# Optimization experiments

Measured on AMD Instinct MI355X. Metric: run time of the kernel, lower is better.

The kernel has to match this reference:

```python
import jax, jax.numpy as jnp
import numpy as np

N_NODES = 100000
N_EDGES = 1600000
IN_CH = 128
OUT_CH = 128
HEADS = 4
HEAD_DIM = OUT_CH // HEADS
NEG_SLOPE_ATT = 0.2   # GATConv default negative_slope
NEG_SLOPE_ACT = 0.2   # block's LeakyReLU(0.2)
BN_EPS = 1e-5


def setup_inputs() -> dict:
    key = jax.random.key(0)
    ks = jax.random.split(key, 6)
    x = jax.random.normal(ks[0], (N_NODES, IN_CH), dtype=jnp.float32)
    edge_index = jax.random.randint(ks[1], (2, N_EDGES), 0, N_NODES, dtype=jnp.int64)
    W = jax.random.normal(ks[2], (IN_CH, HEADS * HEAD_DIM), dtype=jnp.float32) * (1.0 / np.sqrt(IN_CH))
    att_src = jax.random.normal(ks[3], (HEADS, HEAD_DIM), dtype=jnp.float32) * 0.1
    att_dst = jax.random.normal(ks[4], (HEADS, HEAD_DIM), dtype=jnp.float32) * 0.1
    bias = jnp.zeros((OUT_CH,), dtype=jnp.float32)
    gamma = jnp.ones((OUT_CH,), dtype=jnp.float32)
    beta = jnp.zeros((OUT_CH,), dtype=jnp.float32)
    return {"x": x, "edge_index": edge_index, "W": W, "att_src": att_src,
            "att_dst": att_dst, "bias": bias, "gamma": gamma, "beta": beta}


def reference(x, edge_index, W, att_src, att_dst, bias, gamma, beta):
    N = x.shape[0]
    H, C = att_src.shape
    src, dst = edge_index[0], edge_index[1]

    # linear projection per head: [N, H, C]
    h = (x @ W).reshape(N, H, C)

    # per-node attention contributions (alpha_src[i] + alpha_dst[j] on edges)
    a_src = jnp.einsum('nhc,hc->nh', h, att_src)  # [N, H]
    a_dst = jnp.einsum('nhc,hc->nh', h, att_dst)  # [N, H]

    # per-edge raw score, leaky relu (GAT attention nonlinearity)
    e = jax.nn.leaky_relu(a_src[src] + a_dst[dst], NEG_SLOPE_ATT)  # [E, H]

    # segment softmax over edges grouped by destination node
    e_max = jax.ops.segment_max(e, dst, num_segments=N)            # [N, H]
    e_max = jnp.where(jnp.isfinite(e_max), e_max, 0.0)
    ex = jnp.exp(e - e_max[dst])                                   # [E, H]
    denom = jax.ops.segment_sum(ex, dst, num_segments=N)           # [N, H]
    alpha = ex / (denom[dst] + 1e-16)                              # [E, H]

    # scatter-add aggregation of alpha-weighted source features
    msg = alpha[:, :, None] * h[src]                               # [E, H, C]
    out = jax.ops.segment_sum(msg, dst, num_segments=N)            # [N, H, C]
    out = out.reshape(N, H * C) + bias                             # concat heads + bias

    # BatchNorm1d (training mode: batch statistics, biased variance)
    mu = out.mean(axis=0)
    var = out.var(axis=0)
    out = (out - mu) * jax.lax.rsqrt(var + BN_EPS) * gamma + beta

    return jax.nn.leaky_relu(out, NEG_SLOPE_ACT)
```

## Files before the change

### kernel.cpp

```cpp
#include <hip/hip_runtime.h>
#include <hip/hip_fp16.h>
#include <math.h>


#define WAVE  64
#define SHIFT 8
#define CAP   4608
#define CPAD  16

__device__ __forceinline__ float4 leaky4(float4 v, float s) {
    v.x = v.x > 0.f ? v.x : s * v.x;
    v.y = v.y > 0.f ? v.y : s * v.y;
    v.z = v.z > 0.f ? v.z : s * v.z;
    v.w = v.w > 0.f ? v.w : s * v.w;
    return v;
}

__global__ __launch_bounds__(256) void k_gemm_att(
    const float* __restrict__ x, const float* __restrict__ W,
    const float* __restrict__ att_src, const float* __restrict__ att_dst,
    __half* __restrict__ h16, float* __restrict__ a_src, float* __restrict__ a_dst,
    int N)
{
    __shared__ float xsT[128][36];
    __shared__ float Wl[64][128];

    const int t = threadIdx.x;
    const int row0 = blockIdx.x * 32;

    {
        const int r  = t >> 3;
        const int k0 = (t & 7) * 16;
        const int rr = min(row0 + r, N - 1);
        const float4* xp = (const float4*)(x + (size_t)rr * 128 + k0);
        float4 v0 = xp[0], v1 = xp[1], v2 = xp[2], v3 = xp[3];
        float tmp[16] = {v0.x,v0.y,v0.z,v0.w, v1.x,v1.y,v1.z,v1.w,
                         v2.x,v2.y,v2.z,v2.w, v3.x,v3.y,v3.z,v3.w};
        #pragma unroll
        for (int i = 0; i < 16; ++i) xsT[k0 + i][r] = tmp[i];
    }

    const int tx = t & 31;
    const int ty = t >> 5;
    float acc[4][4] = {{0.f}};

    for (int kt = 0; kt < 2; ++kt) {
        __syncthreads();
        {
            const float4* wp = (const float4*)(W + kt * 64 * 128);
            float4* wl = (float4*)&Wl[0][0];
            #pragma unroll
            for (int i = 0; i < 8; ++i) wl[t + 256 * i] = wp[t + 256 * i];
        }
        __syncthreads();
        #pragma unroll
        for (int k = 0; k < 64; ++k) {
            float4 wv = *(const float4*)&Wl[k][tx * 4];
            float4 xv = *(const float4*)&xsT[kt * 64 + k][ty * 4];
            float xa[4] = {xv.x, xv.y, xv.z, xv.w};
            float wa[4] = {wv.x, wv.y, wv.z, wv.w};
            #pragma unroll
            for (int i = 0; i < 4; ++i)
                #pragma unroll
                for (int j = 0; j < 4; ++j)
                    acc[i][j] = fmaf(xa[i], wa[j], acc[i][j]);
        }
    }

    const int head = tx >> 3;
    const float4 s4 = *(const float4*)&att_src[head * 32 + (tx & 7) * 4];
    const float4 d4 = *(const float4*)&att_dst[head * 32 + (tx & 7) * 4];

    #pragma unroll
    for (int i = 0; i < 4; ++i) {
        const int n = row0 + ty * 4 + i;
        if (n < N) {
            union { __half2 h2[2]; uint2 u; } pk;
            pk.h2[0] = __floats2half2_rn(acc[i][0], acc[i][1]);
            pk.h2[1] = __floats2half2_rn(acc[i][2], acc[i][3]);
            *(uint2*)(h16 + (size_t)n * 128 + tx * 4) = pk.u;
        }
        float ss = acc[i][0]*s4.x + acc[i][1]*s4.y + acc[i][2]*s4.z + acc[i][3]*s4.w;
        float dd = acc[i][0]*d4.x + acc[i][1]*d4.y + acc[i][2]*d4.z + acc[i][3]*d4.w;
        #pragma unroll
        for (int off = 1; off < 8; off <<= 1) {
            ss += __shfl_xor(ss, off);
            dd += __shfl_xor(dd, off);
        }
        if ((tx & 7) == 0 && n < N) {
            a_src[n * 4 + head] = ss;
            a_dst[n * 4 + head] = dd;
        }
    }
}

__global__ __launch_bounds__(256) void k_bucket(
    const int* __restrict__ src, const int* __restrict__ dst,
    int* __restrict__ cursor, int2* __restrict__ pairs, int E, int nbkt)
{
    __shared__ int hist[512];
    __shared__ int lcur[512];
    const int t = threadIdx.x;
    hist[t] = 0; hist[t + 256] = 0;
    __syncthreads();

    const int base = blockIdx.x * 2048;
    int sr[8], dr[8];
    #pragma unroll
    for (int i = 0; i < 8; ++i) {
        const int e = base + i * 256 + t;
        if (e < E) { sr[i] = src[e]; dr[i] = dst[e]; }
        else       { sr[i] = -1;     dr[i] = -1; }
    }
    #pragma unroll
    for (int i = 0; i < 8; ++i)
        if (dr[i] >= 0) atomicAdd(&hist[dr[i] >> SHIFT], 1);
    __syncthreads();

    for (int b = t; b < nbkt; b += 256) {
        const int hcount = hist[b];
        lcur[b] = (hcount > 0) ? atomicAdd(&cursor[b * CPAD], hcount) + b * CAP
                               : b * CAP;
    }
    __syncthreads();

    #pragma unroll
    for (int i = 0; i < 8; ++i) {
        if (dr[i] >= 0) {
            const int b = dr[i] >> SHIFT;
            const int pos = atomicAdd(&lcur[b], 1);
            if (pos < b * CAP + CAP)
                pairs[pos] = make_int2(sr[i], dr[i]);
        }
    }
}

__global__ __launch_bounds__(256) void k_fine(
    const int* __restrict__ cursor, const int2* __restrict__ pairs,
    int* __restrict__ offsets, int* __restrict__ deg,
    int* __restrict__ perm_src, int N)
{
    __shared__ int cnt[256];
    __shared__ int scn[256];
    __shared__ int cur[256];

    const int t = threadIdx.x;
    const int b = blockIdx.x;
    const int cnt_b = min(cursor[b * CPAD], CAP);
    const int pbase = b * CAP;

    cnt[t] = 0;
    __syncthreads();

    for (int i = t; i < cnt_b; i += 256) {
        const int2 p = pairs[pbase + i];
        atomicAdd(&cnt[p.y & 255], 1);
    }
    __syncthreads();

    const int v = cnt[t];
    scn[t] = v;
    __syncthreads();
    for (int off = 1; off < 256; off <<= 1) {
        const int add = (t >= off) ? scn[t - off] : 0;
        __syncthreads();
        scn[t] += add;
        __syncthreads();
    }
    const int excl = scn[t] - v;

    const int node = (b << SHIFT) + t;
    if (node < N) {
        offsets[node] = pbase + excl;
        deg[node]     = v;
    }
    cur[t] = pbase + excl;
    __syncthreads();

    for (int i = t; i < cnt_b; i += 256) {
        const int2 p = pairs[pbase + i];
        const int pos = atomicAdd(&cur[p.y & 255], 1);
        perm_src[pos] = p.x;
    }
}

__global__ __launch_bounds__(256) void k_aggregate(
    const int* __restrict__ offsets, const int* __restrict__ deg,
    const int* __restrict__ perm_src,
    const float* __restrict__ a_src, const float* __restrict__ a_dst,
    const __half* __restrict__ h16, float* __restrict__ out, int N)
{
    __shared__ int    ls_s [4][2][32];
    __shared__ float4 ls_ex[4][2][32];

    const int wv   = threadIdx.x >> 6;
    const int lane = threadIdx.x & 63;
    const int nd   = lane >> 5;
    const int l32  = lane & 31;
    const int n    = blockIdx.x * 8 + wv * 2 + nd;
    const bool valid = (n < N);

    const int beg = valid ? offsets[n] : 0;
    const int dg  = valid ? deg[n]     : 0;
    const float4 ad = valid ? *(const float4*)(a_dst + n * 4)
                            : make_float4(0.f, 0.f, 0.f, 0.f);

    const int ph  = (lane >> 4) & 1;
    const int l16 = lane & 15;
    const int ch  = l16 * 8;
    const int hd  = l16 >> 2;
    float acc[8] = {0.f,0.f,0.f,0.f,0.f,0.f,0.f,0.f};
    float dsum = 0.f;

    const int dgmax = max(dg, __shfl_xor(dg, 32));

    for (int base = 0; base < dgmax; base += 32) {
        const int idx = base + l32;
        int s = 0;
        float4 ex = make_float4(0.f, 0.f, 0.f, 0.f);
        if (idx < dg) {
            s = perm_src[beg + idx];
            float4 as = *(const float4*)(a_src + s * 4);
            float4 e = leaky4(make_float4(as.x+ad.x, as.y+ad.y, as.z+ad.z, as.w+ad.w), 0.2f);
            ex.x = __expf(e.x); ex.y = __expf(e.y);
            ex.z = __expf(e.z); ex.w = __expf(e.w);
        }
        ls_s [wv][nd][l32] = s;
        ls_ex[wv][nd][l32] = ex;

        int cn = dg - base;
        cn = (cn < 0) ? 0 : ((cn > 32) ? 32 : cn);
        const int cnmax = max(cn, __shfl_xor(cn, 32));
        const int cnr = (cnmax + 3) & ~3;

        #pragma unroll 2
        for (int t = 0; t < cnr; t += 2) {
            const int slot = t + ph;
            const int   sj  = ls_s[wv][nd][slot];
            const float exj = ((const float*)&ls_ex[wv][nd][slot])[hd];
            union { uint4 u; __half2 h2[4]; } pk;
            pk.u = *(const uint4*)(h16 + (size_t)sj * 128 + ch);
            acc[0] = fmaf(__low2float (pk.h2[0]), exj, acc[0]);
            acc[1] = fmaf(__high2float(pk.h2[0]), exj, acc[1]);
            acc[2] = fmaf(__low2float (pk.h2[1]), exj, acc[2]);
            acc[3] = fmaf(__high2float(pk.h2[1]), exj, acc[3]);
            acc[4] = fmaf(__low2float (pk.h2[2]), exj, acc[4]);
            acc[5] = fmaf(__high2float(pk.h2[2]), exj, acc[5]);
            acc[6] = fmaf(__low2float (pk.h2[3]), exj, acc[6]);
            acc[7] = fmaf(__high2float(pk.h2[3]), exj, acc[7]);
            dsum += exj;
        }
    }

    #pragma unroll
    for (int c = 0; c < 8; ++c) acc[c] += __shfl_xor(acc[c], 16);
    dsum += __shfl_xor(dsum, 16);

    if (ph == 0 && valid) {
        const float inv = 1.0f / (dsum + 1e-16f);
        float* op = out + (size_t)n * 128 + ch;
        *(float4*)(op)     = make_float4(acc[0]*inv, acc[1]*inv, acc[2]*inv, acc[3]*inv);
        *(float4*)(op + 4) = make_float4(acc[4]*inv, acc[5]*inv, acc[6]*inv, acc[7]*inv);
    }
}

__global__ __launch_bounds__(256) void k_bnstats(const float* __restrict__ out,
                                                 float* __restrict__ sums, int N)
{
    const int c    = threadIdx.x & 127;
    const int half = threadIdx.x >> 7;
    float s = 0.f, sq = 0.f;
    for (int r = blockIdx.x * 2 + half; r < N; r += gridDim.x * 2) {
        float v = out[(size_t)r * 128 + c];
        s += v;
        sq = fmaf(v, v, sq);
    }
    __shared__ float ls[256], lq[256];
    ls[threadIdx.x] = s; lq[threadIdx.x] = sq;
    __syncthreads();
    if (half == 0) {
        s  += ls[threadIdx.x + 128];
        sq += lq[threadIdx.x + 128];
        atomicAdd(&sums[c], s);
        atomicAdd(&sums[128 + c], sq);
    }
}

__global__ __launch_bounds__(256) void k_bnapply(float* __restrict__ out,
                                                 const float* __restrict__ sums,
                                                 const float* __restrict__ gamma,
                                                 const float* __restrict__ beta,
                                                 int N)
{
    const int i = blockIdx.x * 256 + threadIdx.x;
    const int total = N * 128;
    if (i >= total) return;
    const int c = i & 127;
    const float invN = 1.0f / (float)N;
    float mu  = sums[c] * invN;
    float var = sums[128 + c] * invN - mu * mu;
    float v = out[i];
    float y = (v - mu) * rsqrtf(var + 1e-5f) * gamma[c] + beta[c];
    out[i] = y > 0.f ? y : 0.2f * y;
}

extern "C" void kernel_launch(void* const* d_in, const int* in_sizes, int n_in,
                              void* d_out, int out_size, void* d_ws, size_t ws_size,
                              hipStream_t stream)
{
    const float* x     = (const float*)d_in[0];
    const int*   ei    = (const int*)  d_in[1];
    const float* W     = (const float*)d_in[2];
    const float* att_s = (const float*)d_in[3];
    const float* att_d = (const float*)d_in[4];
    const float* gamma = (const float*)d_in[6];
    const float* beta  = (const float*)d_in[7];
    float* out = (float*)d_out;

    const int N = in_sizes[0] / 128;
    const int E = in_sizes[1] / 2;
    const int nbkt = (N + (1 << SHIFT) - 1) >> SHIFT;

    char* ws = (char*)d_ws;
    size_t off = 0;
    auto carve = [&](size_t bytes) {
        char* p = ws + off;
        off += (bytes + 255) & ~(size_t)255;
        return p;
    };
    __half* h16      = (__half*)carve((size_t)N * 128 * 2);
    float* a_src     = (float*)carve((size_t)N * 4 * 4);
    float* a_dst     = (float*)carve((size_t)N * 4 * 4);
    int*   offsets   = (int*)  carve((size_t)N * 4);
    int*   deg       = (int*)  carve((size_t)N * 4);
    int*   cursor    = (int*)  carve((size_t)nbkt * CPAD * 4);
    float* bn_sums   = (float*)carve(256 * 4);
    int2*  pairs     = (int2*) carve((size_t)nbkt * CAP * 8);
    int*   perm_src  = (int*)  carve((size_t)nbkt * CAP * 4);

    hipMemsetAsync(cursor, 0, (size_t)nbkt * CPAD * 4, stream);
    hipMemsetAsync(bn_sums, 0, 256 * 4, stream);

    k_gemm_att<<<(N + 31) / 32, 256, 0, stream>>>(x, W, att_s, att_d, h16, a_src, a_dst, N);
    k_bucket<<<(E + 2047) / 2048, 256, 0, stream>>>(ei, ei + E, cursor, pairs, E, nbkt);
    k_fine<<<nbkt, 256, 0, stream>>>(cursor, pairs, offsets, deg, perm_src, N);
    k_aggregate<<<(N + 7) / 8, 256, 0, stream>>>(offsets, deg, perm_src, a_src, a_dst, h16, out, N);
    k_bnstats<<<512, 256, 0, stream>>>(out, bn_sums, N);
    k_bnapply<<<(N * 128 + 255) / 256, 256, 0, stream>>>(out, bn_sums, gamma, beta, N);
}
```

Before: 345.6 us.

## Pack bucket pairs into 32-bit words, stage in LDS, fold memsets into kernels

Bucketed edge pairs are packed into one int each (source id in the low 20 bits, local destination in the high bits), which halves the pairs buffer traffic. k_fine now runs 512 threads, loads each bucket into shared memory once and reuses it for the second pass instead of reading global memory twice. The two hipMemsetAsync calls are removed: cursor is zeroed by block 0 of the GEMM kernel and bn_sums by block 0 of k_fine. The packing assumes node ids fit in 20 bits, and the cursor zeroing in k_gemm_att relies on that kernel finishing before k_bucket starts.

```diff
diff --git a/kernel.cpp b/kernel.cpp
--- a/kernel.cpp
+++ b/kernel.cpp
@@ -7,6 +7,7 @@
 #define SHIFT 8
 #define CAP   4608
 #define CPAD  16
+#define FBLK  512
 
 __device__ __forceinline__ float4 leaky4(float4 v, float s) {
     v.x = v.x > 0.f ? v.x : s * v.x;
@@ -20,13 +21,17 @@
     const float* __restrict__ x, const float* __restrict__ W,
     const float* __restrict__ att_src, const float* __restrict__ att_dst,
     __half* __restrict__ h16, float* __restrict__ a_src, float* __restrict__ a_dst,
-    int N)
+    int* __restrict__ cursor, int czero, int N)
 {
     __shared__ float xsT[128][36];
     __shared__ float Wl[64][128];
 
     const int t = threadIdx.x;
     const int row0 = blockIdx.x * 32;
+
+    if (blockIdx.x == 0) {
+        for (int i = t; i < czero; i += 256) cursor[i] = 0;
+    }
 
     {
         const int r  = t >> 3;
@@ -96,7 +101,7 @@
 
 __global__ __launch_bounds__(256) void k_bucket(
     const int* __restrict__ src, const int* __restrict__ dst,
-    int* __restrict__ cursor, int2* __restrict__ pairs, int E, int nbkt)
+    int* __restrict__ cursor, int* __restrict__ pairs, int E, int nbkt)
 {
     __shared__ int hist[512];
     __shared__ int lcur[512];
@@ -130,57 +135,63 @@
             const int b = dr[i] >> SHIFT;
             const int pos = atomicAdd(&lcur[b], 1);
             if (pos < b * CAP + CAP)
-                pairs[pos] = make_int2(sr[i], dr[i]);
-        }
-    }
-}
-
-__global__ __launch_bounds__(256) void k_fine(
-    const int* __restrict__ cursor, const int2* __restrict__ pairs,
+                pairs[pos] = sr[i] | ((dr[i] & 255) << 20);
+        }
+    }
+}
+
+__global__ __launch_bounds__(FBLK) void k_fine(
+    const int* __restrict__ cursor, const int* __restrict__ pairs,
     int* __restrict__ offsets, int* __restrict__ deg,
-    int* __restrict__ perm_src, int N)
-{
+    int* __restrict__ perm_src, float* __restrict__ bn_sums, int N)
+{
+    __shared__ int stage[CAP];
     __shared__ int cnt[256];
     __shared__ int scn[256];
     __shared__ int cur[256];
 
     const int t = threadIdx.x;
     const int b = blockIdx.x;
+
+    if (b == 0 && t < 256) bn_sums[t] = 0.f;
+
     const int cnt_b = min(cursor[b * CPAD], CAP);
     const int pbase = b * CAP;
 
-    cnt[t] = 0;
-    __syncthreads();
-
-    for (int i = t; i < cnt_b; i += 256) {
-        const int2 p = pairs[pbase + i];
-        atomicAdd(&cnt[p.y & 255], 1);
-    }
-    __syncthreads();
-
-    const int v = cnt[t];
-    scn[t] = v;
+    if (t < 256) cnt[t] = 0;
+    __syncthreads();
+
+    for (int i = t; i < cnt_b; i += FBLK) {
+        const int v = pairs[pbase + i];
+        stage[i] = v;
+        atomicAdd(&cnt[v >> 20], 1);
+    }
+    __syncthreads();
+
+    const int v0 = (t < 256) ? cnt[t] : 0;
+    if (t < 256) scn[t] = v0;
     __syncthreads();
     for (int off = 1; off < 256; off <<= 1) {
-        const int add = (t >= off) ? scn[t - off] : 0;
+        const int add = (t < 256 && t >= off) ? scn[t - off] : 0;
         __syncthreads();
-        scn[t] += add;
+        if (t < 256) scn[t] += add;
         __syncthreads();
     }
-    const int excl = scn[t] - v;
-
-    const int node = (b << SHIFT) + t;
-    if (node < N) {
-        offsets[node] = pbase + excl;
-        deg[node]     = v;
-    }
-    cur[t] = pbase + excl;
-    __syncthreads();
-
-    for (int i = t; i < cnt_b; i += 256) {
-        const int2 p = pairs[pbase + i];
-        const int pos = atomicAdd(&cur[p.y & 255], 1);
-        perm_src[pos] = p.x;
+    if (t < 256) {
+        const int excl = scn[t] - v0;
+        const int node = (b << SHIFT) + t;
+        if (node < N) {
+            offsets[node] = pbase + excl;
+            deg[node]     = v0;
+        }
+        cur[t] = pbase + excl;
+    }
+    __syncthreads();
+
+    for (int i = t; i < cnt_b; i += FBLK) {
+        const int v = stage[i];
+        const int pos = atomicAdd(&cur[v >> 20], 1);
+        perm_src[pos] = v & 0xFFFFF;
     }
 }
 
@@ -335,15 +346,13 @@
     int*   deg       = (int*)  carve((size_t)N * 4);
     int*   cursor    = (int*)  carve((size_t)nbkt * CPAD * 4);
     float* bn_sums   = (float*)carve(256 * 4);
-    int2*  pairs     = (int2*) carve((size_t)nbkt * CAP * 8);
+    int*   pairs     = (int*)  carve((size_t)nbkt * CAP * 4);
     int*   perm_src  = (int*)  carve((size_t)nbkt * CAP * 4);
 
-    hipMemsetAsync(cursor, 0, (size_t)nbkt * CPAD * 4, stream);
-    hipMemsetAsync(bn_sums, 0, 256 * 4, stream);
-
-    k_gemm_att<<<(N + 31) / 32, 256, 0, stream>>>(x, W, att_s, att_d, h16, a_src, a_dst, N);
+    k_gemm_att<<<(N + 31) / 32, 256, 0, stream>>>(x, W, att_s, att_d, h16, a_src, a_dst,
+                                                  cursor, nbkt * CPAD, N);
     k_bucket<<<(E + 2047) / 2048, 256, 0, stream>>>(ei, ei + E, cursor, pairs, E, nbkt);
-    k_fine<<<nbkt, 256, 0, stream>>>(cursor, pairs, offsets, deg, perm_src, N);
+    k_fine<<<nbkt, FBLK, 0, stream>>>(cursor, pairs, offsets, deg, perm_src, bn_sums, N);
     k_aggregate<<<(N + 7) / 8, 256, 0, stream>>>(offsets, deg, perm_src, a_src, a_dst, h16, out, N);
     k_bnstats<<<512, 256, 0, stream>>>(out, bn_sums, N);
     k_bnapply<<<(N * 128 + 255) / 256, 256, 0, stream>>>(out, bn_sums, gamma, beta, N);
```

Result: no change. 339.7 us (-1.7%).
